# Kernel tuning notes

Measured on AMD Instinct MI355X. Metric: run time of the kernel, lower is better.

Reference implementation:

```python
import jax, jax.numpy as jnp
import numpy as np

H = 64; W = 64; P = 16; NPH = 4; NPW = 4; PH = 16; PW = 16; ZD = 32; HD = 1024; UD = 3; B = 256


def affine_grid(theta, Ho, Wo):
    # torch F.affine_grid, align_corners=False. theta [N,2,3] -> grid [N,Ho,Wo,2]
    xs = (2.0 * jnp.arange(Wo, dtype=theta.dtype) + 1.0) / Wo - 1.0
    ys = (2.0 * jnp.arange(Ho, dtype=theta.dtype) + 1.0) / Ho - 1.0
    X, Y = jnp.meshgrid(xs, ys)  # [Ho,Wo] each, x varies along last axis
    base = jnp.stack([X, Y, jnp.ones_like(X)], axis=-1)  # [Ho,Wo,3]
    return jnp.einsum('nij,hwj->nhwi', theta, base)


def grid_sample(img, grid):
    # torch F.grid_sample bilinear, padding_mode='zeros', align_corners=False
    # img [N,H,W], grid [N,Ho,Wo,2] in [-1,1]
    Hi, Wi = img.shape[1], img.shape[2]
    x = (grid[..., 0] + 1.0) * Wi / 2.0 - 0.5
    y = (grid[..., 1] + 1.0) * Hi / 2.0 - 0.5
    x0 = jnp.floor(x); y0 = jnp.floor(y)
    wx = x - x0; wy = y - y0

    def gather(ix, iy):
        valid = (ix >= 0) & (ix < Wi) & (iy >= 0) & (iy < Hi)
        ixc = jnp.clip(ix, 0, Wi - 1).astype(jnp.int32)
        iyc = jnp.clip(iy, 0, Hi - 1).astype(jnp.int32)
        v = jax.vmap(lambda im, yy, xx: im[yy, xx])(img, iyc, ixc)
        return jnp.where(valid, v, 0.0)

    return (gather(x0, y0) * (1 - wx) * (1 - wy)
            + gather(x0 + 1, y0) * wx * (1 - wy)
            + gather(x0, y0 + 1) * (1 - wx) * wy
            + gather(x0 + 1, y0 + 1) * wx * wy)


def rot_tr(u):
    # rotTrMatrix: u [N,3] (angle, tx, ty) -> [N,2,3]
    c = jnp.cos(u[:, 0]); s = jnp.sin(u[:, 0])
    R = jnp.stack([jnp.stack([c, -s], -1), jnp.stack([s, c], -1)], -2)  # [N,2,2]
    return jnp.concatenate([R, u[:, 1:3, None]], axis=2)


def anchor_theta():
    # anchor_move: identity rotation + per-part grid-cell-center translations
    tx = (np.arange(NPW) * (W / NPW) + W / NPW / 2) / W - 0.5
    ty = (np.arange(NPH) * (H / NPH) + H / NPH / 2) / H - 0.5
    th = np.tile(np.concatenate([np.eye(2), np.zeros((2, 1))], axis=1)[None], (P, 1, 1)).astype(np.float32)
    for k in range(P):
        th[k, 0, 2] = tx[k % NPW]
        th[k, 1, 2] = ty[k // NPW]
    return jnp.asarray(th)


def forward(inputs, W1, b1, W2, b2, Wum, bum, Wuv, buv, Wgm, bgm, Wgv, bgv, Wz, M, eps_u, eps_g):
    hid = jax.nn.relu(inputs.reshape(-1, H * W) @ W1 + b1)
    hid = jax.nn.relu(hid @ W2 + b2)
    # global transform distribution (note: F.threshold(x,-6,6) -> 6 where x<=-6)
    gmu = jnp.tanh(hid @ Wgm + bgm)
    gpre = hid @ Wgv + bgv
    gvar = jnp.exp(jnp.where(gpre > -6.0, gpre, 6.0))
    gu = gmu + gvar * eps_g  # sample_u uses mu + var*eps (var, not std) as in source
    # per-part transform distribution (F.threshold(x,-6,-6) -> clamp below at -6)
    umu = jnp.tanh(hid @ Wum + bum)
    upre = hid @ Wuv + buv
    uvar = jnp.exp(jnp.where(upre > -6.0, upre, -6.0))
    u = (umu + uvar * eps_u).reshape(-1, UD)  # [B*P,3]
    # decode parts (input is ones, as in source)
    parts = jax.nn.sigmoid(jnp.ones((B, ZD), inputs.dtype) @ Wz).reshape(B * P, PH, PW)
    padh = (H - PH) // 2; padw = (W - PW) // 2
    parts = jnp.pad(parts, ((0, 0), (padh, H - PH - padh), (padw, W - PW - padw)))
    # anchor placement of parts and kernel masks
    th_a = jnp.tile(anchor_theta(), (B, 1, 1))  # [B*P,2,3], part-minor ordering
    g_a = affine_grid(th_a, H, W)
    parts = grid_sample(parts, g_a)                     # [B*P,H,W]
    KM = grid_sample(M[:B * P].reshape(B * P, H, W), g_a)
    # per-part rotation+translation for parts; translation-only for kernel
    theta = rot_tr(u)                                   # [B*P,2,3]
    g = affine_grid(theta, H, W)
    eye = jnp.broadcast_to(jnp.eye(2, dtype=theta.dtype), (B * P, 2, 2))
    theta_K = jnp.concatenate([eye, theta[:, :, 2:3]], axis=2)
    g_K = affine_grid(theta_K, H, W)
    KM = grid_sample(KM, g_K).reshape(B, P, H, W)
    xp = grid_sample(parts, g).reshape(B, P, H, W)
    # masked weighted compositing
    num = jnp.sum(xp * KM, axis=1)
    den = jnp.sum(KM, axis=1)
    den = jnp.where(den == 0.0, 1.0, den)
    x = num / den
    # global transform
    theta_g = rot_tr(gu)
    g_g = affine_grid(theta_g, H, W)
    return grid_sample(x, g_g)[:, None]  # [B,1,H,W]


def setup_inputs() -> dict:
    key = jax.random.key(0)
    ks = jax.random.split(key, 18)

    def lin(k, fin, fout):
        return jax.random.normal(k, (fin, fout), jnp.float32) / np.sqrt(fin)

    return {
        'inputs': jax.random.uniform(ks[0], (B, H * W), jnp.float32),
        'W1': lin(ks[1], H * W, HD), 'b1': jnp.zeros((HD,), jnp.float32),
        'W2': lin(ks[2], HD, HD), 'b2': jnp.zeros((HD,), jnp.float32),
        'Wum': lin(ks[3], HD, P * UD), 'bum': jnp.zeros((P * UD,), jnp.float32),
        'Wuv': lin(ks[4], HD, P * UD), 'buv': jnp.zeros((P * UD,), jnp.float32),
        'Wgm': lin(ks[5], HD, UD), 'bgm': jnp.zeros((UD,), jnp.float32),
        'Wgv': lin(ks[6], HD, UD), 'bgv': jnp.zeros((UD,), jnp.float32),
        'Wz': lin(ks[7], ZD, P * PH * PW),
        'M': jax.random.uniform(ks[8], (B * P, 1, H, W), jnp.float32),
        'eps_u': jax.random.normal(ks[9], (B, P * UD), jnp.float32),
        'eps_g': jax.random.normal(ks[10], (B, UD), jnp.float32),
    }


def reference(inputs, W1, b1, W2, b2, Wum, bum, Wuv, buv, Wgm, bgm, Wgv, bgv, Wz, M, eps_u, eps_g):
    return forward(inputs, W1, b1, W2, b2, Wum, bum, Wuv, buv, Wgm, bgm, Wgv, bgv, Wz, M, eps_u, eps_g)
```

## Files before the change

### kernel.cpp

```cpp
#include <hip/hip_runtime.h>
#include <math.h>

#define SPLITK 8
#define PSUM_STRIDE 262144

typedef __bf16 bf16x8 __attribute__((ext_vector_type(8)));
typedef float  f32x16 __attribute__((ext_vector_type(16)));

__device__ __forceinline__ unsigned short bf16rne(float x) {
    unsigned int u = __float_as_uint(x);
    unsigned int r = u + 0x7FFFu + ((u >> 16) & 1u);
    return (unsigned short)(r >> 16);
}
__device__ __forceinline__ float bf16tof(unsigned short h) {
    return __uint_as_float(((unsigned int)h) << 16);
}

__global__ __launch_bounds__(256) void prepA(
    const float* __restrict__ inputs, const float* __restrict__ W1,
    unsigned short* __restrict__ Ahi, unsigned short* __restrict__ Alo,
    unsigned short* __restrict__ W1Thi, unsigned short* __restrict__ W1Tlo)
{
    __shared__ float t[32][33];
    int bid = blockIdx.x;
    int tid = threadIdx.x;
    if (bid < 4096) {
        int n0 = (bid & 31) * 32, k0 = (bid >> 5) * 32;
        int c = tid & 31, r0 = tid >> 5;
#pragma unroll
        for (int i = 0; i < 4; i++)
            t[r0 + 8 * i][c] = W1[(size_t)(k0 + r0 + 8 * i) * 1024 + n0 + c];
        __syncthreads();
        int kk = tid & 31, n1 = tid >> 5;
#pragma unroll
        for (int i = 0; i < 4; i++) {
            float x = t[kk][n1 + 8 * i];
            unsigned short h = bf16rne(x);
            unsigned short l = bf16rne(x - bf16tof(h));
            size_t o = (size_t)(n0 + n1 + 8 * i) * 4096 + k0 + kk;
            W1Thi[o] = h;
            W1Tlo[o] = l;
        }
    } else {
        int id = ((bid - 4096) * 256 + tid) * 4;
        float4 x = *(const float4*)(inputs + id);
        ushort4 h, l;
        h.x = bf16rne(x.x); l.x = bf16rne(x.x - bf16tof(h.x));
        h.y = bf16rne(x.y); l.y = bf16rne(x.y - bf16tof(h.y));
        h.z = bf16rne(x.z); l.z = bf16rne(x.z - bf16tof(h.z));
        h.w = bf16rne(x.w); l.w = bf16rne(x.w - bf16tof(h.w));
        *(ushort4*)(Ahi + id) = h;
        *(ushort4*)(Alo + id) = l;
    }
}

__global__ __launch_bounds__(256) void gemm_bf16x3(
    const unsigned short* __restrict__ Ahi, const unsigned short* __restrict__ Alo,
    const unsigned short* __restrict__ Bhi, const unsigned short* __restrict__ Blo,
    float* __restrict__ psum, int K, int kchunk)
{
    __shared__ unsigned short Ah[4096], Al[4096], Bh[4096], Bl[4096];
    int tid = threadIdx.x;
    int n0 = blockIdx.x * 64, m0 = blockIdx.y * 64;
    int kb = blockIdx.z * kchunk;
    int wid = tid >> 6, lane = tid & 63;
    int wm = wid & 1, wn = wid >> 1;
    int lr = lane & 31, hi = lane >> 5;

    int r0 = tid >> 3, ch0 = tid & 7;
    int r1 = (tid + 256) >> 3, ch1 = (tid + 256) & 7;
    int l0 = r0 * 64 + 8 * (ch0 ^ (r0 & 7));
    int l1 = r1 * 64 + 8 * (ch1 ^ (r1 & 7));
    size_t ga0 = (size_t)(m0 + r0) * K + kb + ch0 * 8;
    size_t ga1 = (size_t)(m0 + r1) * K + kb + ch1 * 8;
    size_t gb0 = (size_t)(n0 + r0) * K + kb + ch0 * 8;
    size_t gb1 = (size_t)(n0 + r1) * K + kb + ch1 * 8;

    f32x16 acc_hh = {}, acc_hl = {}, acc_lh = {};

    int nkt = kchunk >> 6;
    uint4 vah0, vah1, val0, val1, vbh0, vbh1, vbl0, vbl1;
    vah0 = *(const uint4*)(Ahi + ga0);
    vah1 = *(const uint4*)(Ahi + ga1);
    val0 = *(const uint4*)(Alo + ga0);
    val1 = *(const uint4*)(Alo + ga1);
    vbh0 = *(const uint4*)(Bhi + gb0);
    vbh1 = *(const uint4*)(Bhi + gb1);
    vbl0 = *(const uint4*)(Blo + gb0);
    vbl1 = *(const uint4*)(Blo + gb1);

    int basea = (wm * 32 + lr) * 64;
    int baseb = (wn * 32 + lr) * 64;
    int sw = lr & 7;

    for (int kt = 0; kt < nkt; kt++) {
        __syncthreads();
        *(uint4*)(Ah + l0) = vah0;
        *(uint4*)(Ah + l1) = vah1;
        *(uint4*)(Al + l0) = val0;
        *(uint4*)(Al + l1) = val1;
        *(uint4*)(Bh + l0) = vbh0;
        *(uint4*)(Bh + l1) = vbh1;
        *(uint4*)(Bl + l0) = vbl0;
        *(uint4*)(Bl + l1) = vbl1;
        __syncthreads();
        if (kt + 1 < nkt) {
            size_t o = (size_t)(kt + 1) * 64;
            vah0 = *(const uint4*)(Ahi + ga0 + o);
            vah1 = *(const uint4*)(Ahi + ga1 + o);
            val0 = *(const uint4*)(Alo + ga0 + o);
            val1 = *(const uint4*)(Alo + ga1 + o);
            vbh0 = *(const uint4*)(Bhi + gb0 + o);
            vbh1 = *(const uint4*)(Bhi + gb1 + o);
            vbl0 = *(const uint4*)(Blo + gb0 + o);
            vbl1 = *(const uint4*)(Blo + gb1 + o);
        }
#pragma unroll
        for (int s = 0; s < 4; s++) {
            int cidx = 8 * (((s << 1) + hi) ^ sw);
            bf16x8 afh = *(const bf16x8*)(Ah + basea + cidx);
            bf16x8 afl = *(const bf16x8*)(Al + basea + cidx);
            bf16x8 bfh = *(const bf16x8*)(Bh + baseb + cidx);
            bf16x8 bfl = *(const bf16x8*)(Bl + baseb + cidx);
            acc_hh = __builtin_amdgcn_mfma_f32_32x32x16_bf16(afh, bfh, acc_hh, 0, 0, 0);
            acc_hl = __builtin_amdgcn_mfma_f32_32x32x16_bf16(afh, bfl, acc_hl, 0, 0, 0);
            acc_lh = __builtin_amdgcn_mfma_f32_32x32x16_bf16(afl, bfh, acc_lh, 0, 0, 0);
        }
    }

    float* op = psum + (size_t)blockIdx.z * PSUM_STRIDE;
    int colg = n0 + wn * 32 + lr;
#pragma unroll
    for (int r = 0; r < 16; r++) {
        int rowl = (r & 3) + 8 * (r >> 2) + 4 * hi;
        op[(size_t)(m0 + wm * 32 + rowl) * 1024 + colg] = acc_hh[r] + acc_hl[r] + acc_lh[r];
    }
}

__global__ __launch_bounds__(256) void reduce_plus(
    const float* __restrict__ psum, const float* __restrict__ bias,
    unsigned short* __restrict__ hi, unsigned short* __restrict__ lo,
    const float* __restrict__ W2,
    unsigned short* __restrict__ W2Thi, unsigned short* __restrict__ W2Tlo,
    const float* __restrict__ Wum, const float* __restrict__ Wuv,
    const float* __restrict__ Wgm, const float* __restrict__ Wgv,
    const float* __restrict__ Wz,
    float* __restrict__ WT, float* __restrict__ partsb)
{
    __shared__ float t[32][33];
    int bid = blockIdx.x;
    int tid = threadIdx.x;
    if (bid < 256) {
        int i = (bid * 256 + tid) * 4;
        float4 v = *(const float4*)(psum + i);
#pragma unroll
        for (int s = 1; s < SPLITK; s++) {
            float4 tt = *(const float4*)(psum + (size_t)s * PSUM_STRIDE + i);
            v.x += tt.x; v.y += tt.y; v.z += tt.z; v.w += tt.w;
        }
        float4 bb = *(const float4*)(bias + (i & 1023));
        v.x = fmaxf(v.x + bb.x, 0.f);
        v.y = fmaxf(v.y + bb.y, 0.f);
        v.z = fmaxf(v.z + bb.z, 0.f);
        v.w = fmaxf(v.w + bb.w, 0.f);
        ushort4 h, l;
        h.x = bf16rne(v.x); l.x = bf16rne(v.x - bf16tof(h.x));
        h.y = bf16rne(v.y); l.y = bf16rne(v.y - bf16tof(h.y));
        h.z = bf16rne(v.z); l.z = bf16rne(v.z - bf16tof(h.z));
        h.w = bf16rne(v.w); l.w = bf16rne(v.w - bf16tof(h.w));
        *(ushort4*)(hi + i) = h;
        *(ushort4*)(lo + i) = l;
    } else if (bid < 1280) {
        int b2 = bid - 256;
        int n0 = (b2 & 31) * 32, k0 = (b2 >> 5) * 32;
        int c = tid & 31, r0 = tid >> 5;
#pragma unroll
        for (int i = 0; i < 4; i++)
            t[r0 + 8 * i][c] = W2[(size_t)(k0 + r0 + 8 * i) * 1024 + n0 + c];
        __syncthreads();
        int kk = tid & 31, n1 = tid >> 5;
#pragma unroll
        for (int i = 0; i < 4; i++) {
            float x = t[kk][n1 + 8 * i];
            unsigned short h = bf16rne(x);
            unsigned short l = bf16rne(x - bf16tof(h));
            size_t o = (size_t)(n0 + n1 + 8 * i) * 1024 + k0 + kk;
            W2Thi[o] = h;
            W2Tlo[o] = l;
        }
    } else if (bid < 1688) {
        int id = (bid - 1280) * 256 + tid;
        int o = id >> 10;
        int k = id & 1023;
        float v;
        if (o < 48)       v = Wum[k * 48 + o];
        else if (o < 96)  v = Wuv[k * 48 + (o - 48)];
        else if (o < 99)  v = Wgm[k * 3 + (o - 96)];
        else              v = Wgv[k * 3 + (o - 99)];
        WT[id] = v;
    } else {
        int idx = (bid - 1688) * 256 + tid;
        float s = 0.f;
#pragma unroll
        for (int z = 0; z < 32; z++) s += Wz[z * 4096 + idx];
        partsb[idx] = 1.f / (1.f + expf(-s));
    }
}

__global__ __launch_bounds__(512) void composite_half(
    const float* __restrict__ psum, const float* __restrict__ b2,
    const float* __restrict__ WT,
    const float* __restrict__ bum, const float* __restrict__ buv,
    const float* __restrict__ bgm, const float* __restrict__ bgv,
    const float* __restrict__ eps_u, const float* __restrict__ eps_g,
    const float* __restrict__ M, const float* __restrict__ parts,
    float* __restrict__ xl_out, float* __restrict__ gu_out)
{
    __shared__ float patch[4096];
    __shared__ float plane[2][4096];
    __shared__ float h2[1024];
    __shared__ float u_raw[51];
    __shared__ float pc[16], psn[16], ptx[16], pty[16], pwx[16], pwy[16];
    __shared__ int pix[16], piy[16];
    int bx = blockIdx.x;
    int b = bx & 255, hf = bx >> 8;
    int tid = threadIdx.x;

#pragma unroll
    for (int e = 0; e < 2; e++) {
        int idx = tid + e * 512;
        float v = psum[(size_t)b * 1024 + idx];
#pragma unroll
        for (int s = 1; s < SPLITK; s++)
            v += psum[(size_t)s * PSUM_STRIDE + (size_t)b * 1024 + idx];
        h2[idx] = fmaxf(v + b2[idx], 0.f);
    }
    for (int i = tid; i < 4096; i += 512) patch[i] = parts[i];
    __syncthreads();

    {
        int w = tid >> 6, l = tid & 63;
        const float4* h4 = (const float4*)h2;
        float4 hr0 = h4[l], hr1 = h4[64 + l], hr2 = h4[128 + l], hr3 = h4[192 + l];
        for (int o = w; o < 51; o += 8) {
            int rm = (o < 48) ? o : (48 + o);
            int rv = (o < 48) ? (o + 48) : (51 + o);
            const float* wpm = WT + rm * 1024 + l * 4;
            const float* wpv = WT + rv * 1024 + l * 4;
            float4 wm0 = *(const float4*)(wpm);
            float4 wm1 = *(const float4*)(wpm + 256);
            float4 wm2 = *(const float4*)(wpm + 512);
            float4 wm3 = *(const float4*)(wpm + 768);
            float4 wv0 = *(const float4*)(wpv);
            float4 wv1 = *(const float4*)(wpv + 256);
            float4 wv2 = *(const float4*)(wpv + 512);
            float4 wv3 = *(const float4*)(wpv + 768);
            float am = 0.f, av = 0.f;
            am = fmaf(hr0.x, wm0.x, am); am = fmaf(hr0.y, wm0.y, am);
            am = fmaf(hr0.z, wm0.z, am); am = fmaf(hr0.w, wm0.w, am);
            av = fmaf(hr0.x, wv0.x, av); av = fmaf(hr0.y, wv0.y, av);
            av = fmaf(hr0.z, wv0.z, av); av = fmaf(hr0.w, wv0.w, av);
            am = fmaf(hr1.x, wm1.x, am); am = fmaf(hr1.y, wm1.y, am);
            am = fmaf(hr1.z, wm1.z, am); am = fmaf(hr1.w, wm1.w, am);
            av = fmaf(hr1.x, wv1.x, av); av = fmaf(hr1.y, wv1.y, av);
            av = fmaf(hr1.z, wv1.z, av); av = fmaf(hr1.w, wv1.w, av);
            am = fmaf(hr2.x, wm2.x, am); am = fmaf(hr2.y, wm2.y, am);
            am = fmaf(hr2.z, wm2.z, am); am = fmaf(hr2.w, wm2.w, am);
            av = fmaf(hr2.x, wv2.x, av); av = fmaf(hr2.y, wv2.y, av);
            av = fmaf(hr2.z, wv2.z, av); av = fmaf(hr2.w, wv2.w, av);
            am = fmaf(hr3.x, wm3.x, am); am = fmaf(hr3.y, wm3.y, am);
            am = fmaf(hr3.z, wm3.z, am); am = fmaf(hr3.w, wm3.w, am);
            av = fmaf(hr3.x, wv3.x, av); av = fmaf(hr3.y, wv3.y, av);
            av = fmaf(hr3.z, wv3.z, av); av = fmaf(hr3.w, wv3.w, av);
#pragma unroll
            for (int s = 32; s; s >>= 1) {
                am += __shfl_xor(am, s, 64);
                av += __shfl_xor(av, s, 64);
            }
            if (l == 0) {
                if (o < 48) {
                    float umu = tanhf(am + bum[o]);
                    float uvar = expf(fmaxf(av + buv[o], -6.f));
                    u_raw[o] = umu + uvar * eps_u[b * 48 + o];
                } else {
                    int n = o - 48;
                    float gmu = tanhf(am + bgm[n]);
                    float gpre = av + bgv[n];
                    float gvar = expf(gpre > -6.f ? gpre : 6.f);
                    float gv = gmu + gvar * eps_g[b * 3 + n];
                    u_raw[o] = gv;
                    gu_out[b * 3 + n] = gv;
                }
            }
        }
    }
    __syncthreads();

    if (tid < 16) {
        float ang = u_raw[tid * 3 + 0];
        float tx = u_raw[tid * 3 + 1], ty = u_raw[tid * 3 + 2];
        pc[tid] = cosf(ang);
        psn[tid] = sinf(ang);
        ptx[tid] = tx;
        pty[tid] = ty;
        float ax = fminf(fmaxf(32.f * tx, -16384.f), 16384.f);
        float fax = floorf(ax);
        pwx[tid] = ax - fax;
        pix[tid] = (int)fax;
        float ay = fminf(fmaxf(32.f * ty, -16384.f), 16384.f);
        float fay = floorf(ay);
        pwy[tid] = ay - fay;
        piy[tid] = (int)fay;
    }
    const float* Mb = M + ((size_t)(b * 16) << 12);
    ((float4*)plane[0])[tid] = ((const float4*)Mb)[tid];
    ((float4*)plane[0])[tid + 512] = ((const float4*)Mb)[tid + 512];
    float4 pf0 = ((const float4*)(Mb + 4096))[tid];
    float4 pf1 = ((const float4*)(Mb + 4096))[tid + 512];
    __syncthreads();

    int j = tid & 63;
    int i0 = hf * 32 + (tid >> 6) * 4;
    float xnv = (float)(2 * j + 1) * (1.f / 64.f) - 1.f;
    float ynv0 = (float)(2 * i0 + 1) * (1.f / 64.f) - 1.f;

    float num[4] = {}, den[4] = {};
    float* pl_cur = plane[0];
    float* pl_nxt = plane[1];

    for (int p = 0; p < 16; p++) {
        if (p + 1 < 16) {
            ((float4*)pl_nxt)[tid] = pf0;
            ((float4*)pl_nxt)[tid + 512] = pf1;
        }
        if (p + 2 < 16) {
            pf0 = ((const float4*)(Mb + ((size_t)(p + 2) << 12)))[tid];
            pf1 = ((const float4*)(Mb + ((size_t)(p + 2) << 12)))[tid + 512];
        }

        int dx = 8 * (p & 3) - 12;
        int dy = 8 * (p >> 2) - 12;
        float c = pc[p], s = psn[p], tx = ptx[p], ty = pty[p];
        float wx = pwx[p], wy = pwy[p];
        int ix = pix[p], iy = piy[p];
        int iY = iy + dy;

        int x0 = j + ix;
        int X = x0 + dx;
        bool vc0 = ((unsigned)x0 < 64u) && ((unsigned)X < 64u);
        bool vc1 = ((unsigned)(x0 + 1) < 64u) && ((unsigned)(X + 1) < 64u);
        float w0 = vc0 ? (1.f - wx) : 0.f;
        float w1 = vc1 ? wx : 0.f;
        int Xc0 = min(max(X, 0), 63);
        int Xc1 = min(max(X + 1, 0), 63);

        const float* pl = pl_cur;
        float R[5];
#pragma unroll
        for (int r = 0; r < 5; r++) {
            int i = i0 + r;
            int ri = i + iY;
            bool vr = ((unsigned)(i + iy) < 64u) && ((unsigned)ri < 64u);
            int ric = min(max(ri, 0), 63);
            const float* row = pl + (ric << 6);
            float val = fmaf(w0, row[Xc0], w1 * row[Xc1]);
            R[r] = vr ? val : 0.f;
        }

        float gx0 = fmaf(-s, ynv0, fmaf(c, xnv, tx));
        float gy0 = fmaf(c, ynv0, fmaf(s, xnv, ty));
        float xs = fmaf(gx0, 32.f, 31.5f);
        float ysv = fmaf(gy0, 32.f, 31.5f);
        int ox = 24 - dx, oy = 24 - dy;
        float oxf = (float)ox, oyf = (float)oy;
        const float* pp = patch + (p << 8);
#pragma unroll
        for (int r = 0; r < 4; r++) {
            float km = fmaf(wy, R[r + 1] - R[r], R[r]);
            den[r] += km;

            if (xs >= oxf - 1.f && xs < oxf + 16.f &&
                ysv >= oyf - 1.f && ysv < oyf + 16.f) {
                float xf = floorf(xs), yf = floorf(ysv);
                float wxx = xs - xf, wyy = ysv - yf;
                int a0 = (int)yf - oy;
                int b0c = (int)xf - ox;
                float v00 = 0.f, v10 = 0.f, v01 = 0.f, v11 = 0.f;
                if ((unsigned)a0 < 16u) {
                    const float* pr = pp + a0 * 16;
                    if ((unsigned)b0c < 16u) v00 = pr[b0c];
                    if ((unsigned)(b0c + 1) < 16u) v10 = pr[b0c + 1];
                }
                if ((unsigned)(a0 + 1) < 16u) {
                    const float* pr = pp + (a0 + 1) * 16;
                    if ((unsigned)b0c < 16u) v01 = pr[b0c];
                    if ((unsigned)(b0c + 1) < 16u) v11 = pr[b0c + 1];
                }
                float top = fmaf(wxx, v10 - v00, v00);
                float bot = fmaf(wxx, v11 - v01, v01);
                float xp = fmaf(wyy, bot - top, top);
                num[r] = fmaf(xp, km, num[r]);
            }
            xs -= s;
            ysv += c;
        }
        __syncthreads();
        float* tmp = pl_cur; pl_cur = pl_nxt; pl_nxt = tmp;
    }

    float* xo = xl_out + ((size_t)b << 12);
#pragma unroll
    for (int r = 0; r < 4; r++) {
        float d = (den[r] == 0.f) ? 1.f : den[r];
        xo[(i0 + r) * 64 + j] = num[r] / d;
    }
}

__global__ __launch_bounds__(1024) void final_transform(
    const float* __restrict__ xl_in, const float* __restrict__ gu,
    float* __restrict__ out)
{
    __shared__ float xl[4096];
    int b = blockIdx.x;
    int tid = threadIdx.x;
    ((float4*)xl)[tid] = ((const float4*)(xl_in + ((size_t)b << 12)))[tid];
    __syncthreads();

    int j = tid & 63;
    int i0 = (tid >> 6) * 4;
    float xnv = (float)(2 * j + 1) * (1.f / 64.f) - 1.f;

    float ang = gu[b * 3 + 0], gtx = gu[b * 3 + 1], gty = gu[b * 3 + 2];
    float cg = cosf(ang), sg = sinf(ang);
    float* ob = out + ((size_t)b << 12);
#pragma unroll
    for (int r = 0; r < 4; r++) {
        int i = i0 + r;
        float ynv = (float)(2 * i + 1) * (1.f / 64.f) - 1.f;
        float gx = cg * xnv - sg * ynv + gtx;
        float gy = sg * xnv + cg * ynv + gty;
        gx = fminf(fmaxf(gx, -8.f), 8.f);
        gy = fminf(fmaxf(gy, -8.f), 8.f);
        float xs = fmaf(gx, 32.f, 31.5f);
        float ysv = fmaf(gy, 32.f, 31.5f);
        float xf = floorf(xs), yf = floorf(ysv);
        float wx = xs - xf, wy = ysv - yf;
        int x0 = (int)xf, y0 = (int)yf;
        float v00 = 0.f, v10 = 0.f, v01 = 0.f, v11 = 0.f;
        bool vx0 = (unsigned)x0 < 64u, vx1 = (unsigned)(x0 + 1) < 64u;
        if ((unsigned)y0 < 64u) {
            const float* row = xl + y0 * 64;
            if (vx0) v00 = row[x0];
            if (vx1) v10 = row[x0 + 1];
        }
        if ((unsigned)(y0 + 1) < 64u) {
            const float* row = xl + (y0 + 1) * 64;
            if (vx0) v01 = row[x0];
            if (vx1) v11 = row[x0 + 1];
        }
        float top = fmaf(wx, v10 - v00, v00);
        float bot = fmaf(wx, v11 - v01, v01);
        ob[i * 64 + j] = fmaf(wy, bot - top, top);
    }
}

extern "C" void kernel_launch(void* const* d_in, const int* in_sizes, int n_in,
                              void* d_out, int out_size, void* d_ws, size_t ws_size,
                              hipStream_t stream)
{
    (void)in_sizes; (void)n_in; (void)out_size; (void)ws_size;
    const float* inputs = (const float*)d_in[0];
    const float* W1  = (const float*)d_in[1];
    const float* b1  = (const float*)d_in[2];
    const float* W2  = (const float*)d_in[3];
    const float* b2  = (const float*)d_in[4];
    const float* Wum = (const float*)d_in[5];
    const float* bum = (const float*)d_in[6];
    const float* Wuv = (const float*)d_in[7];
    const float* buv = (const float*)d_in[8];
    const float* Wgm = (const float*)d_in[9];
    const float* bgm = (const float*)d_in[10];
    const float* Wgv = (const float*)d_in[11];
    const float* bgv = (const float*)d_in[12];
    const float* Wz  = (const float*)d_in[13];
    const float* Mm  = (const float*)d_in[14];
    const float* eps_u = (const float*)d_in[15];
    const float* eps_g = (const float*)d_in[16];

    float* ws = (float*)d_ws;
    float* psum      = ws;
    float* parts_buf = psum + 8 * PSUM_STRIDE;
    float* WTh_buf   = parts_buf + 4096;
    unsigned short* us = (unsigned short*)(WTh_buf + 104448);
    unsigned short* Ahi   = us;
    unsigned short* Alo   = Ahi + 1048576;
    unsigned short* W1Thi = Alo + 1048576;
    unsigned short* W1Tlo = W1Thi + 4194304;
    unsigned short* W2Thi = W1Tlo + 4194304;
    unsigned short* W2Tlo = W2Thi + 1048576;
    unsigned short* H1hi  = W2Tlo + 1048576;
    unsigned short* H1lo  = H1hi + 262144;
    float* xl_buf = (float*)(H1lo + 262144);
    float* gu_buf = xl_buf + 1048576;

    prepA<<<5120, 256, 0, stream>>>(inputs, W1, Ahi, Alo, W1Thi, W1Tlo);

    gemm_bf16x3<<<dim3(16, 4, SPLITK), 256, 0, stream>>>(Ahi, Alo, W1Thi, W1Tlo,
                                                         psum, 4096, 4096 / SPLITK);
    reduce_plus<<<1704, 256, 0, stream>>>(psum, b1, H1hi, H1lo,
                                          W2, W2Thi, W2Tlo,
                                          Wum, Wuv, Wgm, Wgv, Wz,
                                          WTh_buf, parts_buf);
    gemm_bf16x3<<<dim3(16, 4, SPLITK), 256, 0, stream>>>(H1hi, H1lo, W2Thi, W2Tlo,
                                                         psum, 1024, 1024 / SPLITK);
    composite_half<<<512, 512, 0, stream>>>(psum, b2, WTh_buf, bum, buv,
                                            bgm, bgv, eps_u, eps_g,
                                            Mm, parts_buf, xl_buf, gu_buf);
    final_transform<<<256, 1024, 0, stream>>>(xl_buf, gu_buf, (float*)d_out);
}
```

Baseline: 204.9 us.

## Fuse composite and final transform into one kernel reading M from global

```diff
diff --git a/kernel.cpp b/kernel.cpp
--- a/kernel.cpp
+++ b/kernel.cpp
@@ -207,42 +207,41 @@
     }
 }
 
-__global__ __launch_bounds__(512) void composite_half(
+__global__ __launch_bounds__(1024) void composite_direct(
     const float* __restrict__ psum, const float* __restrict__ b2,
     const float* __restrict__ WT,
     const float* __restrict__ bum, const float* __restrict__ buv,
     const float* __restrict__ bgm, const float* __restrict__ bgv,
     const float* __restrict__ eps_u, const float* __restrict__ eps_g,
     const float* __restrict__ M, const float* __restrict__ parts,
-    float* __restrict__ xl_out, float* __restrict__ gu_out)
+    float* __restrict__ out)
 {
     __shared__ float patch[4096];
-    __shared__ float plane[2][4096];
+    __shared__ float xl[4096];
     __shared__ float h2[1024];
     __shared__ float u_raw[51];
     __shared__ float pc[16], psn[16], ptx[16], pty[16], pwx[16], pwy[16];
     __shared__ int pix[16], piy[16];
-    int bx = blockIdx.x;
-    int b = bx & 255, hf = bx >> 8;
+    int b = blockIdx.x;
     int tid = threadIdx.x;
 
-#pragma unroll
-    for (int e = 0; e < 2; e++) {
-        int idx = tid + e * 512;
-        float v = psum[(size_t)b * 1024 + idx];
+    const float* Mb = M + ((size_t)(b * 16) << 12);
+
+    {
+        float v = psum[(size_t)b * 1024 + tid];
 #pragma unroll
         for (int s = 1; s < SPLITK; s++)
-            v += psum[(size_t)s * PSUM_STRIDE + (size_t)b * 1024 + idx];
-        h2[idx] = fmaxf(v + b2[idx], 0.f);
-    }
-    for (int i = tid; i < 4096; i += 512) patch[i] = parts[i];
+            v += psum[(size_t)s * PSUM_STRIDE + (size_t)b * 1024 + tid];
+        h2[tid] = fmaxf(v + b2[tid], 0.f);
+    }
+    for (int i = tid; i < 4096; i += 1024) patch[i] = parts[i];
     __syncthreads();
 
     {
         int w = tid >> 6, l = tid & 63;
         const float4* h4 = (const float4*)h2;
         float4 hr0 = h4[l], hr1 = h4[64 + l], hr2 = h4[128 + l], hr3 = h4[192 + l];
-        for (int o = w; o < 51; o += 8) {
+        for (int o = w; o < 51; o += 16) {
             int rm = (o < 48) ? o : (48 + o);
             int rv = (o < 48) ? (o + 48) : (51 + o);
             const float* wpm = WT + rm * 1024 + l * 4;
@@ -287,9 +286,7 @@
                     float gmu = tanhf(am + bgm[n]);
                     float gpre = av + bgv[n];
                     float gvar = expf(gpre > -6.f ? gpre : 6.f);
-                    float gv = gmu + gvar * eps_g[b * 3 + n];
-                    u_raw[o] = gv;
-                    gu_out[b * 3 + n] = gv;
+                    u_raw[o] = gmu + gvar * eps_g[b * 3 + n];
                 }
             }
         }
@@ -312,32 +309,16 @@
         pwy[tid] = ay - fay;
         piy[tid] = (int)fay;
     }
-    const float* Mb = M + ((size_t)(b * 16) << 12);
-    ((float4*)plane[0])[tid] = ((const float4*)Mb)[tid];
-    ((float4*)plane[0])[tid + 512] = ((const float4*)Mb)[tid + 512];
-    float4 pf0 = ((const float4*)(Mb + 4096))[tid];
-    float4 pf1 = ((const float4*)(Mb + 4096))[tid + 512];
     __syncthreads();
 
     int j = tid & 63;
-    int i0 = hf * 32 + (tid >> 6) * 4;
+    int i0 = (tid >> 6) * 4;
     float xnv = (float)(2 * j + 1) * (1.f / 64.f) - 1.f;
     float ynv0 = (float)(2 * i0 + 1) * (1.f / 64.f) - 1.f;
 
     float num[4] = {}, den[4] = {};
-    float* pl_cur = plane[0];
-    float* pl_nxt = plane[1];
 
     for (int p = 0; p < 16; p++) {
-        if (p + 1 < 16) {
-            ((float4*)pl_nxt)[tid] = pf0;
-            ((float4*)pl_nxt)[tid + 512] = pf1;
-        }
-        if (p + 2 < 16) {
-            pf0 = ((const float4*)(Mb + ((size_t)(p + 2) << 12)))[tid];
-            pf1 = ((const float4*)(Mb + ((size_t)(p + 2) << 12)))[tid + 512];
-        }
-
         int dx = 8 * (p & 3) - 12;
         int dy = 8 * (p >> 2) - 12;
         float c = pc[p], s = psn[p], tx = ptx[p], ty = pty[p];
@@ -354,7 +335,7 @@
         int Xc0 = min(max(X, 0), 63);
         int Xc1 = min(max(X + 1, 0), 63);
 
-        const float* pl = pl_cur;
+        const float* pl = Mb + ((size_t)p << 12);
         float R[5];
 #pragma unroll
         for (int r = 0; r < 5; r++) {
@@ -404,33 +385,16 @@
             xs -= s;
             ysv += c;
         }
-        __syncthreads();
-        float* tmp = pl_cur; pl_cur = pl_nxt; pl_nxt = tmp;
-    }
-
-    float* xo = xl_out + ((size_t)b << 12);
+    }
+
 #pragma unroll
     for (int r = 0; r < 4; r++) {
         float d = (den[r] == 0.f) ? 1.f : den[r];
-        xo[(i0 + r) * 64 + j] = num[r] / d;
-    }
-}
-
-__global__ __launch_bounds__(1024) void final_transform(
-    const float* __restrict__ xl_in, const float* __restrict__ gu,
-    float* __restrict__ out)
-{
-    __shared__ float xl[4096];
-    int b = blockIdx.x;
-    int tid = threadIdx.x;
-    ((float4*)xl)[tid] = ((const float4*)(xl_in + ((size_t)b << 12)))[tid];
+        xl[(i0 + r) * 64 + j] = num[r] / d;
+    }
     __syncthreads();
 
-    int j = tid & 63;
-    int i0 = (tid >> 6) * 4;
-    float xnv = (float)(2 * j + 1) * (1.f / 64.f) - 1.f;
-
-    float ang = gu[b * 3 + 0], gtx = gu[b * 3 + 1], gty = gu[b * 3 + 2];
+    float ang = u_raw[48], gtx = u_raw[49], gty = u_raw[50];
     float cg = cosf(ang), sg = sinf(ang);
     float* ob = out + ((size_t)b << 12);
 #pragma unroll
@@ -500,8 +464,6 @@
     unsigned short* W2Tlo = W2Thi + 1048576;
     unsigned short* H1hi  = W2Tlo + 1048576;
     unsigned short* H1lo  = H1hi + 262144;
-    float* xl_buf = (float*)(H1lo + 262144);
-    float* gu_buf = xl_buf + 1048576;
 
     prepA<<<5120, 256, 0, stream>>>(inputs, W1, Ahi, Alo, W1Thi, W1Tlo);
 
@@ -513,8 +475,7 @@
                                           WTh_buf, parts_buf);
     gemm_bf16x3<<<dim3(16, 4, SPLITK), 256, 0, stream>>>(H1hi, H1lo, W2Thi, W2Tlo,
                                                          psum, 1024, 1024 / SPLITK);
-    composite_half<<<512, 512, 0, stream>>>(psum, b2, WTh_buf, bum, buv,
-                                            bgm, bgv, eps_u, eps_g,
-                                            Mm, parts_buf, xl_buf, gu_buf);
-    final_transform<<<256, 1024, 0, stream>>>(xl_buf, gu_buf, (float*)d_out);
-}
+    composite_direct<<<256, 1024, 0, stream>>>(psum, b2, WTh_buf, bum, buv,
+                                               bgm, bgv, eps_u, eps_g,
+                                               Mm, parts_buf, (float*)d_out);
+}
```

Result: faster. 200.6 us (-2.1%).
